# Kernel optimization log

Measured on AMD Instinct MI355X. Metric: run time of the kernel, lower is better.

Reference implementation:

```python
import jax, jax.numpy as jnp
import numpy as np

N = 4096      # nodes
HID = 512     # hidden_size
HEADS = 8
DH = HID // HEADS
EPS = 1e-5    # BatchNorm eps


def setup_inputs() -> dict:
    key = jax.random.key(0)
    ks = jax.random.split(key, 16)
    h = jax.random.normal(ks[0], (N, HID), jnp.float32)
    # sparse adjacency (~degree 32) with self-loops so every row has a neighbor
    A = (jax.random.uniform(ks[1], (N, N)) < 0.008).astype(jnp.float32)
    A = jnp.maximum(A, jnp.eye(N, dtype=jnp.float32))
    w = lambda k, shp: jax.random.normal(k, shp, jnp.float32) * 0.02
    return {
        "A": A, "h": h,
        "Wq": w(ks[2], (HID, HID)), "bq": jnp.zeros((HID,), jnp.float32),
        "Wk": w(ks[3], (HID, HID)), "bk": jnp.zeros((HID,), jnp.float32),
        "Wv": w(ks[4], (HID, HID)), "bv": jnp.zeros((HID,), jnp.float32),
        "Wo": w(ks[5], (HID, HID)), "bo": jnp.zeros((HID,), jnp.float32),
        "bn1_g": jnp.ones((HID,), jnp.float32), "bn1_b": jnp.zeros((HID,), jnp.float32),
        "bn2_g": jnp.ones((HID,), jnp.float32), "bn2_b": jnp.zeros((HID,), jnp.float32),
        "W1": w(ks[6], (HID, 2 * HID)), "b1": jnp.zeros((2 * HID,), jnp.float32),
        "W2": w(ks[7], (2 * HID, HID)), "b2": jnp.zeros((HID,), jnp.float32),
    }


def _batchnorm(x, g, b):
    # BatchNorm1d training mode: stats over the node (batch) axis
    m = jnp.mean(x, axis=0)
    v = jnp.var(x, axis=0)
    return g * (x - m) * jax.lax.rsqrt(v + EPS) + b


def _layer(A, h, Wq, bq, Wk, bk, Wv, bv, Wo, bo,
           bn1_g, bn1_b, bn2_g, bn2_b, W1, b1, W2, b2):
    n = h.shape[0]
    q = (h @ Wq + bq).reshape(n, HEADS, DH)
    k = (h @ Wk + bk).reshape(n, HEADS, DH)
    v = (h @ Wv + bv).reshape(n, HEADS, DH)
    # scores [heads, n, m], masked by adjacency
    scores = jnp.einsum('nhd,mhd->hnm', q, k) / np.float32(np.sqrt(DH))
    scores = jnp.where(A[None, :, :] > 0, scores, jnp.float32(-1e9))
    attn = jax.nn.softmax(scores, axis=-1)
    o = jnp.einsum('hnm,mhd->nhd', attn, v).reshape(n, HID)
    h1 = o @ Wo + bo
    h = _batchnorm(h + h1, bn1_g, bn1_b)
    h2 = jax.nn.relu(h @ W1 + b1) @ W2 + b2
    return _batchnorm(h + h2, bn2_g, bn2_b)


def reference(A, h, Wq, bq, Wk, bk, Wv, bv, Wo, bo,
              bn1_g, bn1_b, bn2_g, bn2_b, W1, b1, W2, b2):
    return _layer(A, h, Wq, bq, Wk, bk, Wv, bv, Wo, bo,
                  bn1_g, bn1_b, bn2_g, bn2_b, W1, b1, W2, b2)
```

## Files before the change

### kernel.cpp

```cpp
#include <hip/hip_runtime.h>

#define N_NODES 4096
#define HID 512
#define HEADS 8
#define DH 64
#define EPS 1e-5f
#define MAXD 128

typedef __attribute__((ext_vector_type(8))) short bf16x8;
typedef __attribute__((ext_vector_type(4))) float f32x4;

__device__ __forceinline__ unsigned short f2bf(float f) {
    unsigned int u = __float_as_uint(f);
    unsigned int r = (u + 0x7FFFu + ((u >> 16) & 1u)) >> 16;
    return (unsigned short)r;
}
__device__ __forceinline__ float blo(unsigned int u) {
    return __uint_as_float(u << 16);
}
__device__ __forceinline__ float bhi(unsigned int u) {
    return __uint_as_float(u & 0xffff0000u);
}

__device__ __forceinline__ void gld_lds16(const void* g, void* l) {
    __builtin_amdgcn_global_load_lds(
        (const __attribute__((address_space(1))) unsigned int*)g,
        (__attribute__((address_space(3))) unsigned int*)l, 16, 0, 0);
}

template<int TM, int EPI, int ADJ>
__global__ __launch_bounds__(256) void gemm_bf16(
    const unsigned short* __restrict__ Xb, const unsigned short* __restrict__ Wt,
    const float* __restrict__ bias, const float* __restrict__ res,
    const unsigned short* __restrict__ resb,
    float* __restrict__ outf, unsigned short* __restrict__ outb,
    float* __restrict__ sum, float* __restrict__ sumsq,
    int K, int Nc,
    const float* __restrict__ Adj, int* __restrict__ adjIdx,
    int* __restrict__ adjCnt)
{
    const int tid = threadIdx.x;

    if (ADJ && blockIdx.z == 1) {
        const int lane = tid & 63;
        const int wv4 = tid >> 6;
        __shared__ int s_cnt[4];
        const unsigned long long lt = (1ull << lane) - 1ull;
        const int nb = gridDim.x * gridDim.y;
        for (int n = blockIdx.y * gridDim.x + blockIdx.x; n < N_NODES; n += nb) {
            const float4* r4 = (const float4*)(Adj + (size_t)n * N_NODES);
            float4 av[4];
            #pragma unroll
            for (int t = 0; t < 4; ++t)
                av[t] = r4[wv4 * 256 + t * 64 + lane];
            int cnt = 0;
            #pragma unroll
            for (int t = 0; t < 4; ++t) {
                #pragma unroll
                for (int b = 0; b < 4; ++b) {
                    float vb = (b == 0) ? av[t].x : (b == 1) ? av[t].y : (b == 2) ? av[t].z : av[t].w;
                    cnt += __popcll(__ballot(vb > 0.0f));
                }
            }
            if (lane == 0) s_cnt[wv4] = cnt;
            __syncthreads();
            int base = 0, total = 0;
            #pragma unroll
            for (int w = 0; w < 4; ++w) {
                if (w < wv4) base += s_cnt[w];
                total += s_cnt[w];
            }
            #pragma unroll
            for (int t = 0; t < 4; ++t) {
                #pragma unroll
                for (int b = 0; b < 4; ++b) {
                    float vb = (b == 0) ? av[t].x : (b == 1) ? av[t].y : (b == 2) ? av[t].z : av[t].w;
                    unsigned long long m = __ballot(vb > 0.0f);
                    if (vb > 0.0f) {
                        int p = base + __popcll(m & lt);
                        if (p < MAXD) adjIdx[n * MAXD + p] = wv4 * 1024 + t * 256 + lane * 4 + b;
                    }
                    base += __popcll(m);
                }
            }
            if (tid == 0) adjCnt[n] = total < MAXD ? total : MAXD;
            __syncthreads();
        }
        return;
    }

    constexpr int WM = TM / 64;
    __shared__ __align__(16) unsigned short As[TM * 64];
    __shared__ __align__(16) unsigned short Bs[64 * 64];

    const int lane = tid & 63;
    const int wv = tid >> 6;
    const int m0 = blockIdx.y * TM, n0 = blockIdx.x * 64;
    const int lc = lane & 15, lq = lane >> 4;
    const int rowbase = wv * (WM * 16);

    const int srow = tid >> 3;
    const int schunk = (tid & 7) ^ (srow & 7);
    unsigned short* ldsA = As + tid * 8;
    unsigned short* ldsB = Bs + tid * 8;
    const int rs0 = lq ^ (lc & 7);
    const int rs1 = (4 + lq) ^ (lc & 7);

    f32x4 acc[WM][4] = {};

    for (int k0 = 0; k0 < K; k0 += 64) {
        const unsigned short* gA = Xb + (size_t)(m0 + srow) * K + k0 + schunk * 8;
        const unsigned short* gB = Wt + (size_t)(n0 + srow) * K + k0 + schunk * 8;
        #pragma unroll
        for (int p = 0; p < TM / 32; ++p)
            gld_lds16(gA + (size_t)(p * 32) * K, ldsA + p * 2048);
        #pragma unroll
        for (int p = 0; p < 2; ++p)
            gld_lds16(gB + (size_t)(p * 32) * K, ldsB + p * 2048);
        __syncthreads();

        #pragma unroll
        for (int hh = 0; hh < 2; ++hh) {
            const int rs = hh ? rs1 : rs0;
            bf16x8 af[WM], bfr[4];
            #pragma unroll
            for (int i = 0; i < WM; ++i)
                af[i] = *(const bf16x8*)&As[(rowbase + i * 16 + lc) * 64 + rs * 8];
            #pragma unroll
            for (int j = 0; j < 4; ++j)
                bfr[j] = *(const bf16x8*)&Bs[(j * 16 + lc) * 64 + rs * 8];
            #pragma unroll
            for (int i = 0; i < WM; ++i)
                #pragma unroll
                for (int j = 0; j < 4; ++j)
                    acc[i][j] = __builtin_amdgcn_mfma_f32_16x16x32_bf16(af[i], bfr[j], acc[i][j], 0, 0, 0);
        }
        __syncthreads();
    }

    float cs[4] = {}, css[4] = {};
    #pragma unroll
    for (int i = 0; i < WM; ++i) {
        #pragma unroll
        for (int j = 0; j < 4; ++j) {
            const int gr0 = m0 + rowbase + i * 16 + lq * 4;
            const int gc = n0 + j * 16 + lc;
            const float bi = bias[gc];
            #pragma unroll
            for (int r = 0; r < 4; ++r) {
                float val = acc[i][j][r] + bi;
                size_t off = (size_t)(gr0 + r) * Nc + gc;
                if (EPI == 0)      outb[off] = f2bf(val);
                else if (EPI == 1) outb[off] = f2bf(fmaxf(val, 0.f));
                else {
                    if (EPI == 2) val += res[off];
                    else          val += blo((unsigned int)resb[off]);
                    outf[off] = val;
                    cs[j] += val; css[j] += val * val;
                }
            }
        }
    }
    if (EPI >= 2) {
        #pragma unroll
        for (int j = 0; j < 4; ++j) {
            float s = cs[j], ss = css[j];
            s += __shfl_xor(s, 16); s += __shfl_xor(s, 32);
            ss += __shfl_xor(ss, 16); ss += __shfl_xor(ss, 32);
            if (lq == 0) {
                const int gc = n0 + j * 16 + lc;
                atomicAdd(&sum[gc], s);
                atomicAdd(&sumsq[gc], ss);
            }
        }
    }
}

__global__ __launch_bounds__(256) void prep_all(
    const float* __restrict__ Wq, const float* __restrict__ Wk,
    const float* __restrict__ Wv, const float* __restrict__ Wo,
    const float* __restrict__ W1, const float* __restrict__ W2,
    const float* __restrict__ h,
    const float* __restrict__ bq, const float* __restrict__ bk,
    const float* __restrict__ bv,
    unsigned short* __restrict__ wqkvT, unsigned short* __restrict__ woT,
    unsigned short* __restrict__ w1T, unsigned short* __restrict__ w2T,
    unsigned int* __restrict__ hb, float* __restrict__ bqkv,
    float* __restrict__ st)
{
    const int z = blockIdx.z;
    if (z < 6) {
        const float* in; unsigned short* out; int R, C;
        switch (z) {
            case 0: in = Wq; out = wqkvT;          R = 512;  C = 512;  break;
            case 1: in = Wk; out = wqkvT + 262144; R = 512;  C = 512;  break;
            case 2: in = Wv; out = wqkvT + 524288; R = 512;  C = 512;  break;
            case 3: in = Wo; out = woT;            R = 512;  C = 512;  break;
            case 4: in = W1; out = w1T;            R = 512;  C = 1024; break;
            default: in = W2; out = w2T;           R = 1024; C = 512;  break;
        }
        const int bc = blockIdx.x * 32, br = blockIdx.y * 32;
        if (bc >= C || br >= R) return;
        __shared__ float tile[32][33];
        const int tx = threadIdx.x & 31, ty = threadIdx.x >> 5;
        #pragma unroll
        for (int r = ty; r < 32; r += 8)
            tile[r][tx] = in[(size_t)(br + r) * C + bc + tx];
        __syncthreads();
        #pragma unroll
        for (int r = ty; r < 32; r += 8)
            out[(size_t)(bc + r) * R + br + tx] = f2bf(tile[tx][r]);
    } else if (z == 6) {
        const int blk = blockIdx.y * 32 + blockIdx.x;
        const int i = blk * 512 + threadIdx.x * 2;
        const float4* in4 = (const float4*)h;
        #pragma unroll
        for (int u = 0; u < 2; ++u) {
            float4 f = in4[i + u];
            hb[(i + u) * 2]     = (unsigned int)f2bf(f.x) | ((unsigned int)f2bf(f.y) << 16);
            hb[(i + u) * 2 + 1] = (unsigned int)f2bf(f.z) | ((unsigned int)f2bf(f.w) << 16);
        }
    } else {
        const int blk = blockIdx.y * 32 + blockIdx.x;
        const int i = blk * 256 + threadIdx.x;
        if (i < 1536) bqkv[i] = i < 512 ? bq[i] : (i < 1024 ? bk[i - 512] : bv[i - 1024]);
        if (i < 2048) st[i] = 0.0f;
    }
}

__global__ __launch_bounds__(256) void sparse_attn6(
    const int* __restrict__ adjIdx, const int* __restrict__ adjCnt,
    const unsigned short* __restrict__ qkv, unsigned short* __restrict__ o)
{
    const int n = blockIdx.x;
    const int tid = threadIdx.x;
    const int wv = tid >> 6, lane = tid & 63;

    __shared__ int s_idx[MAXD];
    __shared__ float s_p[8][MAXD];

    const int d = adjCnt[n];
    if (tid < d) s_idx[tid] = adjIdx[n * MAXD + tid];
    __syncthreads();

    const int jl = lane >> 3;
    const int dgs = lane & 7;
    const int jl2 = lane >> 4;
    const int dga = lane & 15;
    const int h0 = wv, h1 = wv + 4;

    const unsigned short* qp = qkv + (size_t)n * 1536 + dgs * 8;
    uint4 qa = *(const uint4*)(qp + h0 * 64);
    uint4 qb = *(const uint4*)(qp + h1 * 64);
    const float a0 = blo(qa.x), a1 = bhi(qa.x), a2 = blo(qa.y), a3 = bhi(qa.y);
    const float a4 = blo(qa.z), a5 = bhi(qa.z), a6 = blo(qa.w), a7 = bhi(qa.w);
    const float b0 = blo(qb.x), b1 = bhi(qb.x), b2 = blo(qb.y), b3 = bhi(qb.y);
    const float b4 = blo(qb.z), b5 = bhi(qb.z), b6 = blo(qb.w), b7 = bhi(qb.w);

    uint4 ka = {0, 0, 0, 0}, kb = {0, 0, 0, 0};
    if (jl < d) {
        const unsigned short* p = qkv + (size_t)s_idx[jl] * 1536 + 512 + dgs * 8;
        ka = *(const uint4*)(p + h0 * 64);
        kb = *(const uint4*)(p + h1 * 64);
    }
    for (int j0 = 0; j0 < d; j0 += 8) {
        const uint4 ca = ka, cb = kb;
        const int jn = j0 + 8 + jl;
        if (jn < d) {
            const unsigned short* p = qkv + (size_t)s_idx[jn] * 1536 + 512 + dgs * 8;
            ka = *(const uint4*)(p + h0 * 64);
            kb = *(const uint4*)(p + h1 * 64);
        }
        const int jc = j0 + jl;
        float s0 = 0.f, s1 = 0.f;
        if (jc < d) {
            s0 = a0 * blo(ca.x) + a1 * bhi(ca.x) + a2 * blo(ca.y) + a3 * bhi(ca.y)
               + a4 * blo(ca.z) + a5 * bhi(ca.z) + a6 * blo(ca.w) + a7 * bhi(ca.w);
            s1 = b0 * blo(cb.x) + b1 * bhi(cb.x) + b2 * blo(cb.y) + b3 * bhi(cb.y)
               + b4 * blo(cb.z) + b5 * bhi(cb.z) + b6 * blo(cb.w) + b7 * bhi(cb.w);
        }
        s0 += __shfl_xor(s0, 1); s1 += __shfl_xor(s1, 1);
        s0 += __shfl_xor(s0, 2); s1 += __shfl_xor(s1, 2);
        s0 += __shfl_xor(s0, 4); s1 += __shfl_xor(s1, 4);
        if (dgs == 0 && jc < d) {
            s_p[h0][jc] = s0 * 0.125f;
            s_p[h1][jc] = s1 * 0.125f;
        }
    }

    float inv0, inv1;
    #pragma unroll
    for (int hh = 0; hh < 2; ++hh) {
        float* sp = s_p[hh ? h1 : h0];
        float mx = -1e30f;
        for (int j = lane; j < d; j += 64) mx = fmaxf(mx, sp[j]);
        #pragma unroll
        for (int off = 32; off; off >>= 1) mx = fmaxf(mx, __shfl_xor(mx, off));
        float sum = 0.f;
        for (int j = lane; j < d; j += 64) {
            float e = __expf(sp[j] - mx);
            sp[j] = e;
            sum += e;
        }
        #pragma unroll
        for (int off = 32; off; off >>= 1) sum += __shfl_xor(sum, off);
        if (hh) inv1 = 1.0f / sum; else inv0 = 1.0f / sum;
    }

    float x0 = 0.f, x1 = 0.f, x2 = 0.f, x3 = 0.f;
    float y0 = 0.f, y1 = 0.f, y2 = 0.f, y3 = 0.f;
    uint2 va = {0, 0}, vb = {0, 0};
    if (jl2 < d) {
        const unsigned short* p = qkv + (size_t)s_idx[jl2] * 1536 + 1024 + dga * 4;
        va = *(const uint2*)(p + h0 * 64);
        vb = *(const uint2*)(p + h1 * 64);
    }
    for (int j0 = 0; j0 < d; j0 += 4) {
        const uint2 ca = va, cb = vb;
        const int jn = j0 + 4 + jl2;
        if (jn < d) {
            const unsigned short* p = qkv + (size_t)s_idx[jn] * 1536 + 1024 + dga * 4;
            va = *(const uint2*)(p + h0 * 64);
            vb = *(const uint2*)(p + h1 * 64);
        }
        const int jc = j0 + jl2;
        if (jc < d) {
            const float p0 = s_p[h0][jc], p1 = s_p[h1][jc];
            x0 += p0 * blo(ca.x); x1 += p0 * bhi(ca.x);
            x2 += p0 * blo(ca.y); x3 += p0 * bhi(ca.y);
            y0 += p1 * blo(cb.x); y1 += p1 * bhi(cb.x);
            y2 += p1 * blo(cb.y); y3 += p1 * bhi(cb.y);
        }
    }
    x0 += __shfl_xor(x0, 16); x0 += __shfl_xor(x0, 32);
    x1 += __shfl_xor(x1, 16); x1 += __shfl_xor(x1, 32);
    x2 += __shfl_xor(x2, 16); x2 += __shfl_xor(x2, 32);
    x3 += __shfl_xor(x3, 16); x3 += __shfl_xor(x3, 32);
    y0 += __shfl_xor(y0, 16); y0 += __shfl_xor(y0, 32);
    y1 += __shfl_xor(y1, 16); y1 += __shfl_xor(y1, 32);
    y2 += __shfl_xor(y2, 16); y2 += __shfl_xor(y2, 32);
    y3 += __shfl_xor(y3, 16); y3 += __shfl_xor(y3, 32);
    if (jl2 == 0) {
        uint2 w0, w1;
        w0.x = (unsigned int)f2bf(x0 * inv0) | ((unsigned int)f2bf(x1 * inv0) << 16);
        w0.y = (unsigned int)f2bf(x2 * inv0) | ((unsigned int)f2bf(x3 * inv0) << 16);
        w1.x = (unsigned int)f2bf(y0 * inv1) | ((unsigned int)f2bf(y1 * inv1) << 16);
        w1.y = (unsigned int)f2bf(y2 * inv1) | ((unsigned int)f2bf(y3 * inv1) << 16);
        *(uint2*)(o + (size_t)n * 512 + h0 * 64 + dga * 4) = w0;
        *(uint2*)(o + (size_t)n * 512 + h1 * 64 + dga * 4) = w1;
    }
}

__global__ __launch_bounds__(256) void bn_apply4(
    const float4* __restrict__ x, const float* __restrict__ sum,
    const float* __restrict__ sumsq, const float* __restrict__ g,
    const float* __restrict__ b, float4* __restrict__ yf,
    uint2* __restrict__ yb)
{
    const int i = blockIdx.x * 256 + threadIdx.x;
    const int c4 = i & 127;
    const float4 s4 = ((const float4*)sum)[c4];
    const float4 q4 = ((const float4*)sumsq)[c4];
    const float4 g4 = ((const float4*)g)[c4];
    const float4 b4 = ((const float4*)b)[c4];
    const float4 xv = x[i];
    const float kN = 1.0f / N_NODES;
    float4 r;
    { float m = s4.x * kN; r.x = g4.x * (xv.x - m) * rsqrtf(q4.x * kN - m * m + EPS) + b4.x; }
    { float m = s4.y * kN; r.y = g4.y * (xv.y - m) * rsqrtf(q4.y * kN - m * m + EPS) + b4.y; }
    { float m = s4.z * kN; r.z = g4.z * (xv.z - m) * rsqrtf(q4.z * kN - m * m + EPS) + b4.z; }
    { float m = s4.w * kN; r.w = g4.w * (xv.w - m) * rsqrtf(q4.w * kN - m * m + EPS) + b4.w; }
    if (yf) yf[i] = r;
    if (yb) {
        uint2 p;
        p.x = (unsigned int)f2bf(r.x) | ((unsigned int)f2bf(r.y) << 16);
        p.y = (unsigned int)f2bf(r.z) | ((unsigned int)f2bf(r.w) << 16);
        yb[i] = p;
    }
}


extern "C" void kernel_launch(void* const* d_in, const int* in_sizes, int n_in,
                              void* d_out, int out_size, void* d_ws, size_t ws_size,
                              hipStream_t stream)
{
    const float* A   = (const float*)d_in[0];
    const float* h   = (const float*)d_in[1];
    const float* Wq  = (const float*)d_in[2];
    const float* bq  = (const float*)d_in[3];
    const float* Wk  = (const float*)d_in[4];
    const float* bk  = (const float*)d_in[5];
    const float* Wv  = (const float*)d_in[6];
    const float* bv  = (const float*)d_in[7];
    const float* Wo  = (const float*)d_in[8];
    const float* bo  = (const float*)d_in[9];
    const float* g1  = (const float*)d_in[10];
    const float* b1g = (const float*)d_in[11];
    const float* g2  = (const float*)d_in[12];
    const float* b2g = (const float*)d_in[13];
    const float* W1  = (const float*)d_in[14];
    const float* b1  = (const float*)d_in[15];
    const float* W2  = (const float*)d_in[16];
    const float* b2  = (const float*)d_in[17];
    float* out = (float*)d_out;

    float* ws = (float*)d_ws;
    unsigned short* hb    = (unsigned short*)(ws);
    unsigned short* qkvb  = (unsigned short*)(ws + 1048576);
    unsigned short* o_bf  = (unsigned short*)(ws + 4194304);
    unsigned short* wqkvT = (unsigned short*)(ws + 5242880);
    unsigned short* woT   = (unsigned short*)(ws + 5636096);
    unsigned short* w1T   = (unsigned short*)(ws + 5767168);
    unsigned short* w2T   = (unsigned short*)(ws + 6029312);
    unsigned short* t_b   = (unsigned short*)(ws + 6291456);
    float* x1   = ws + 8388608;
    float* x2   = ws + 10485760;
    unsigned short* xb1_b = (unsigned short*)(ws + 12582912);
    float* bqkv = ws + 13631488;
    float* st   = ws + 13633024;
    int* adjIdx = (int*)(ws + 6291456);
    int* adjCnt = (int*)(ws + 6815744);

    prep_all<<<dim3(32, 32, 8), dim3(256), 0, stream>>>(
        Wq, Wk, Wv, Wo, W1, W2, h, bq, bk, bv,
        wqkvT, woT, w1T, w2T, (unsigned int*)hb, bqkv, st);

    gemm_bf16<128, 0, 1><<<dim3(24, 32, 2), dim3(256), 0, stream>>>(
        hb, wqkvT, bqkv, nullptr, nullptr, nullptr, qkvb, nullptr, nullptr,
        512, 1536, A, adjIdx, adjCnt);

    sparse_attn6<<<dim3(N_NODES), dim3(256), 0, stream>>>(adjIdx, adjCnt, qkvb, o_bf);

    gemm_bf16<64, 2, 0><<<dim3(8, 64), dim3(256), 0, stream>>>(
        o_bf, woT, bo, h, nullptr, x1, nullptr, st, st + 512,
        512, 512, nullptr, nullptr, nullptr);

    bn_apply4<<<dim3(2048), dim3(256), 0, stream>>>(
        (const float4*)x1, st, st + 512, g1, b1g, nullptr, (uint2*)xb1_b);

    gemm_bf16<128, 1, 0><<<dim3(16, 32), dim3(256), 0, stream>>>(
        xb1_b, w1T, b1, nullptr, nullptr, nullptr, t_b, nullptr, nullptr,
        512, 1024, nullptr, nullptr, nullptr);

    gemm_bf16<64, 3, 0><<<dim3(8, 64), dim3(256), 0, stream>>>(
        t_b, w2T, b2, nullptr, xb1_b, x2, nullptr, st + 1024, st + 1536,
        1024, 512, nullptr, nullptr, nullptr);

    bn_apply4<<<dim3(2048), dim3(256), 0, stream>>>(
        (const float4*)x2, st + 1024, st + 1536, g2, b2g, (float4*)out, nullptr);

    (void)in_sizes; (void)n_in; (void)out_size; (void)ws_size;
}
```

Measured before the change: 233.3 us.

## Double-buffer LDS tiles in bf16 GEMM to overlap global loads with MFMA

The GEMM main loop now uses two LDS buffers for A and B. The next K-tile is issued through global_load_lds while MFMAs run on the current tile, which is meant to hide global memory latency behind compute. This doubles the LDS footprint per block, which may reduce occupancy. The loop also assumes K/64 is even.

```diff
diff --git a/kernel.cpp b/kernel.cpp
--- a/kernel.cpp
+++ b/kernel.cpp
@@ -26,6 +26,43 @@
     __builtin_amdgcn_global_load_lds(
         (const __attribute__((address_space(1))) unsigned int*)g,
         (__attribute__((address_space(3))) unsigned int*)l, 16, 0, 0);
+}
+
+template<int TM>
+__device__ __forceinline__ void g_stage(
+    const unsigned short* gA, const unsigned short* gB,
+    unsigned short* AsBuf, unsigned short* BsBuf, int tid, int koff, int K)
+{
+    #pragma unroll
+    for (int p = 0; p < TM / 32; ++p)
+        gld_lds16(gA + koff + (size_t)(p * 32) * K, AsBuf + tid * 8 + p * 2048);
+    #pragma unroll
+    for (int p = 0; p < 2; ++p)
+        gld_lds16(gB + koff + (size_t)(p * 32) * K, BsBuf + tid * 8 + p * 2048);
+}
+
+template<int TM>
+__device__ __forceinline__ void g_compute(
+    const unsigned short* AsBuf, const unsigned short* BsBuf,
+    f32x4 (&acc)[TM / 64][4], int rowbase, int lc, int rs0, int rs1)
+{
+    constexpr int WM = TM / 64;
+    #pragma unroll
+    for (int hh = 0; hh < 2; ++hh) {
+        const int rs = hh ? rs1 : rs0;
+        bf16x8 af[WM], bfr[4];
+        #pragma unroll
+        for (int i = 0; i < WM; ++i)
+            af[i] = *(const bf16x8*)&AsBuf[(rowbase + i * 16 + lc) * 64 + rs * 8];
+        #pragma unroll
+        for (int j = 0; j < 4; ++j)
+            bfr[j] = *(const bf16x8*)&BsBuf[(j * 16 + lc) * 64 + rs * 8];
+        #pragma unroll
+        for (int i = 0; i < WM; ++i)
+            #pragma unroll
+            for (int j = 0; j < 4; ++j)
+                acc[i][j] = __builtin_amdgcn_mfma_f32_16x16x32_bf16(af[i], bfr[j], acc[i][j], 0, 0, 0);
+    }
 }
 
 template<int TM, int EPI, int ADJ>
@@ -90,8 +127,8 @@
     }
 
     constexpr int WM = TM / 64;
-    __shared__ __align__(16) unsigned short As[TM * 64];
-    __shared__ __align__(16) unsigned short Bs[64 * 64];
+    __shared__ __align__(16) unsigned short As[2][TM * 64];
+    __shared__ __align__(16) unsigned short Bs[2][64 * 64];
 
     const int lane = tid & 63;
     const int wv = tid >> 6;
@@ -101,40 +138,25 @@
 
     const int srow = tid >> 3;
     const int schunk = (tid & 7) ^ (srow & 7);
-    unsigned short* ldsA = As + tid * 8;
-    unsigned short* ldsB = Bs + tid * 8;
     const int rs0 = lq ^ (lc & 7);
     const int rs1 = (4 + lq) ^ (lc & 7);
 
+    const unsigned short* gA = Xb + (size_t)(m0 + srow) * K + schunk * 8;
+    const unsigned short* gB = Wt + (size_t)(n0 + srow) * K + schunk * 8;
+
     f32x4 acc[WM][4] = {};
 
-    for (int k0 = 0; k0 < K; k0 += 64) {
-        const unsigned short* gA = Xb + (size_t)(m0 + srow) * K + k0 + schunk * 8;
-        const unsigned short* gB = Wt + (size_t)(n0 + srow) * K + k0 + schunk * 8;
-        #pragma unroll
-        for (int p = 0; p < TM / 32; ++p)
-            gld_lds16(gA + (size_t)(p * 32) * K, ldsA + p * 2048);
-        #pragma unroll
-        for (int p = 0; p < 2; ++p)
-            gld_lds16(gB + (size_t)(p * 32) * K, ldsB + p * 2048);
+    g_stage<TM>(gA, gB, As[0], Bs[0], tid, 0, K);
+    __syncthreads();
+
+    const int nt = K >> 6;
+    for (int t = 0; t < nt; t += 2) {
+        g_stage<TM>(gA, gB, As[1], Bs[1], tid, (t + 1) * 64, K);
+        g_compute<TM>(As[0], Bs[0], acc, rowbase, lc, rs0, rs1);
         __syncthreads();
-
-        #pragma unroll
-        for (int hh = 0; hh < 2; ++hh) {
-            const int rs = hh ? rs1 : rs0;
-            bf16x8 af[WM], bfr[4];
-            #pragma unroll
-            for (int i = 0; i < WM; ++i)
-                af[i] = *(const bf16x8*)&As[(rowbase + i * 16 + lc) * 64 + rs * 8];
-            #pragma unroll
-            for (int j = 0; j < 4; ++j)
-                bfr[j] = *(const bf16x8*)&Bs[(j * 16 + lc) * 64 + rs * 8];
-            #pragma unroll
-            for (int i = 0; i < WM; ++i)
-                #pragma unroll
-                for (int j = 0; j < 4; ++j)
-                    acc[i][j] = __builtin_amdgcn_mfma_f32_16x16x32_bf16(af[i], bfr[j], acc[i][j], 0, 0, 0);
-        }
+        if (t + 2 < nt)
+            g_stage<TM>(gA, gB, As[0], Bs[0], tid, (t + 2) * 64, K);
+        g_compute<TM>(As[1], Bs[1], acc, rowbase, lc, rs0, rs1);
         __syncthreads();
     }
 
```

Result: slower. 239.5 us (+2.6%).
